# Kernel optimization log

Measured on AMD Instinct MI355X. Metric: run time of the kernel, lower is better.

## Reference

```python
import jax, jax.numpy as jnp
import numpy as np

T, B, TD, HD, VD = 64, 4096, 512, 256, 484
LN_EPS = 1e-5   # torch nn.LayerNorm default
COS_EPS = 1e-8  # torch F.cosine_similarity default


def setup_inputs() -> dict:
    key = jax.random.key(0)
    ks = jax.random.split(key, 6)
    w = lambda k, shape: jax.random.normal(k, shape, dtype=jnp.float32) * 0.02
    return {
        "t_feat": jax.random.normal(ks[0], (B, TD), dtype=jnp.float32),
        "W1": w(ks[1], (T, HD, TD)),            # torch Linear weight layout [out, in]
        "b1": w(ks[2], (T, HD)),
        "gamma": jnp.ones((T, HD), jnp.float32),
        "beta": jnp.zeros((T, HD), jnp.float32),
        "W2": w(ks[3], (T, VD, HD)),
        "b2": w(ks[4], (T, VD)),
        "centroids": jax.random.normal(ks[5], (T, VD), dtype=jnp.float32),
    }


def reference(t_feat, W1, b1, gamma, beta, W2, b2, centroids):
    # All T per-task mappers batched into one grouped GEMM pipeline.
    # Linear1: [B, TD] x [T, HD, TD] -> [T, B, HD]
    h = jnp.einsum("bd,thd->tbh", t_feat, W1) + b1[:, None, :]
    # LayerNorm over hidden dim (per task affine params)
    mu = jnp.mean(h, axis=-1, keepdims=True)
    var = jnp.mean(jnp.square(h - mu), axis=-1, keepdims=True)
    h = (h - mu) * jax.lax.rsqrt(var + LN_EPS) * gamma[:, None, :] + beta[:, None, :]
    # Exact GELU (torch nn.GELU default uses erf)
    h = jax.nn.gelu(h, approximate=False)
    # Linear2: [T, B, HD] x [T, VD, HD] -> [T, B, VD] predicted visual features
    v = jnp.einsum("tbh,tvh->tbv", h, W2) + b2[:, None, :]
    # Cosine similarity vs each task centroid (eps-clamped norms, as in torch)
    v_norm = jnp.maximum(jnp.linalg.norm(v, axis=-1), COS_EPS)          # [T, B]
    c_norm = jnp.maximum(jnp.linalg.norm(centroids, axis=-1), COS_EPS)  # [T]
    cos = jnp.einsum("tbv,tv->tb", v, centroids) / (v_norm * c_norm[:, None])
    distances = jnp.mean(1.0 - cos, axis=-1)  # [T] mean cosine distance per task
    best_task = jnp.argmin(distances)          # top-1 routing decision
    return distances, best_task
```

## Files before the change

kernel.cpp:

```cpp
#include <hip/hip_runtime.h>
#include <math.h>

#define TASKS 64
#define NB    4096
#define TDI   512
#define HDI   256
#define VDI   484

#define WS_TF   ((size_t)0)
#define WS_W1   ((size_t)4194304)
#define WS_W2   ((size_t)20971520)
#define WS_CN   ((size_t)37748736)
#define WS_BC   ((size_t)37748992)
#define WS_ACC  ((size_t)37749248)

#define LDS_HP 0
#define LDS_B2 32768
#define LDS_R0 34816
#define LDS_R1 35840
#define LDS_MU 36864
#define LDS_RS 37120
#define SMEM_BYTES 37376

typedef _Float16 half8 __attribute__((ext_vector_type(8)));
typedef float    f32x4 __attribute__((ext_vector_type(4)));

#define MFMA16(a, b, c) __builtin_amdgcn_mfma_f32_16x16x32_f16((a), (b), (c), 0, 0, 0)

__device__ __forceinline__ half8 cvt8(float4 v0, float4 v1) {
  half8 r;
  r[0]=(_Float16)v0.x; r[1]=(_Float16)v0.y; r[2]=(_Float16)v0.z; r[3]=(_Float16)v0.w;
  r[4]=(_Float16)v1.x; r[5]=(_Float16)v1.y; r[6]=(_Float16)v1.z; r[7]=(_Float16)v1.w;
  return r;
}

__device__ __forceinline__ float gelu_exact(float x) {
  float az = fabsf(x) * 0.70710678118654752f;
  float d  = fmaf(0.3275911f, az, 1.0f);
  float t; asm("v_rcp_f32 %0, %1" : "=v"(t) : "v"(d));
  float p  = fmaf(t, 1.061405429f, -1.453152027f);
  p = fmaf(t, p, 1.421413741f);
  p = fmaf(t, p, -0.284496736f);
  p = fmaf(t, p, 0.254829592f);
  p = p * t;
  float m = az * az * -1.4426950408889634f;
  float e; asm("v_exp_f32 %0, %1" : "=v"(e) : "v"(m));
  float er = fmaf(-p, e, 1.0f);
  er = copysignf(er, x);
  float hx = 0.5f * x;
  return fmaf(hx, er, hx);
}

extern "C" __global__ void prep_all(const float* __restrict__ t_feat,
                                    const float* __restrict__ W1,
                                    const float* __restrict__ W2,
                                    const float* __restrict__ b2,
                                    const float* __restrict__ cent,
                                    _Float16* __restrict__ tf,
                                    _Float16* __restrict__ w1,
                                    _Float16* __restrict__ w2,
                                    float* __restrict__ cnorm,
                                    float* __restrict__ bc,
                                    float* __restrict__ accum) {
  const int bid = blockIdx.x, tid = threadIdx.x;
  __shared__ float redc[256], redb[256];
  if (bid < 1024) {
    int p = bid * 256 + tid;
    int rb = p >> 12, r = p & 4095;
    int ks = r >> 8, rt = (r >> 6) & 3, q = (r >> 4) & 3, l15 = r & 15;
    int row = rb * 64 + rt * 16 + l15, k8 = ks * 4 + q;
    float4 v0 = ((const float4*)t_feat)[(row * 64 + k8) * 2];
    float4 v1 = ((const float4*)t_feat)[(row * 64 + k8) * 2 + 1];
    *(half8*)(tf + (size_t)p * 8) = cvt8(v0, v1);
  } else if (bid < 5120) {
    int p = (bid - 1024) * 256 + tid;
    int t = p >> 14, r = p & 16383;
    int w_ = r >> 12, ks = (r >> 8) & 15, ct = (r >> 6) & 3, q = (r >> 4) & 3, l15 = r & 15;
    int hd = w_ * 64 + ct * 16 + l15, k8 = ks * 4 + q;
    float4 v0 = ((const float4*)W1)[((size_t)(t * 256 + hd) * 64 + k8) * 2];
    float4 v1 = ((const float4*)W1)[((size_t)(t * 256 + hd) * 64 + k8) * 2 + 1];
    *(half8*)(w1 + (size_t)p * 8) = cvt8(v0, v1);
  } else if (bid < 9216) {
    int p = (bid - 5120) * 256 + tid;
    int t = p >> 14, r = p & 16383;
    int pass = r >> 13, w_ = (r >> 11) & 3, ks = (r >> 8) & 7;
    int ct = (r >> 6) & 3, q = (r >> 4) & 3, l15 = r & 15;
    int vd = pass * 256 + w_ * 64 + ct * 16 + l15, k8 = ks * 4 + q;
    half8 hv;
    if (vd < 484) {
      float4 v0 = ((const float4*)W2)[((size_t)(t * 484 + vd) * 64 + k8 * 2)];
      float4 v1 = ((const float4*)W2)[((size_t)(t * 484 + vd) * 64 + k8 * 2) + 1];
      hv = cvt8(v0, v1);
    } else if (vd >= 485) {
      #pragma unroll
      for (int i = 0; i < 8; ++i) hv[i] = (_Float16)0.f;
    } else {
      return;
    }
    *(half8*)(w2 + (size_t)p * 8) = hv;
  } else {
    int t = bid - 9216;
    int h = tid;
    float wcv = 0.f;
    for (int v = 0; v < VDI; ++v)
      wcv += W2[((size_t)t * VDI + v) * HDI + h] * cent[(size_t)t * VDI + v];
    {
      int ks = h >> 5, q = (h >> 3) & 3;
      size_t o = (size_t)t * 16384 + 8192 + 3 * 2048 + ks * 256 + 2 * 64 + q * 16 + 4;
      w2[o * 8 + (h & 7)] = (_Float16)wcv;
    }
    float c2 = 0.f, b2c = 0.f;
    for (int v = h; v < VDI; v += 256) {
      float c = cent[(size_t)t * VDI + v];
      c2 += c * c;
      b2c += b2[(size_t)t * VDI + v] * c;
    }
    redc[tid] = c2; redb[tid] = b2c;
    __syncthreads();
    if (tid < 64) {
      c2  = redc[tid] + redc[tid + 64] + redc[tid + 128] + redc[tid + 192];
      b2c = redb[tid] + redb[tid + 64] + redb[tid + 128] + redb[tid + 192];
      #pragma unroll
      for (int off = 32; off; off >>= 1) { c2 += __shfl_xor(c2, off); b2c += __shfl_xor(b2c, off); }
      if (tid == 0) { cnorm[t] = sqrtf(c2); bc[t] = b2c; accum[t] = 0.f; }
    }
  }
}


#define STEP_RELOAD(A, ACC, PB) do {                                           \
  __builtin_amdgcn_s_setprio(1);                                               \
  _Pragma("unroll") for (int ct_ = 0; ct_ < 4; ++ct_) {                        \
    ACC[0][ct_] = MFMA16(A[0], b[ct_], ACC[0][ct_]);                           \
    ACC[1][ct_] = MFMA16(A[1], b[ct_], ACC[1][ct_]);                           \
    ACC[2][ct_] = MFMA16(A[2], b[ct_], ACC[2][ct_]);                           \
    ACC[3][ct_] = MFMA16(A[3], b[ct_], ACC[3][ct_]);                           \
    b[ct_] = (PB)[ct_ * 64];                                                   \
  }                                                                            \
  __builtin_amdgcn_s_setprio(0);                                               \
} while (0)

#define STEP_LAST(A, ACC) do {                                                 \
  __builtin_amdgcn_s_setprio(1);                                               \
  _Pragma("unroll") for (int ct_ = 0; ct_ < 4; ++ct_) {                        \
    ACC[0][ct_] = MFMA16(A[0], b[ct_], ACC[0][ct_]);                           \
    ACC[1][ct_] = MFMA16(A[1], b[ct_], ACC[1][ct_]);                           \
    ACC[2][ct_] = MFMA16(A[2], b[ct_], ACC[2][ct_]);                           \
    ACC[3][ct_] = MFMA16(A[3], b[ct_], ACC[3][ct_]);                           \
  }                                                                            \
  __builtin_amdgcn_s_setprio(0);                                               \
} while (0)

#define LD_A4(D, P) do { D[0] = (P)[0]; D[1] = (P)[64]; D[2] = (P)[128]; D[3] = (P)[192]; } while (0)

extern "C" __global__ void __launch_bounds__(256, 4)
router_main(const half8* __restrict__ tfv,
            const half8* __restrict__ w1v,
            const half8* __restrict__ w2v,
            const float* __restrict__ b1,
            const float* __restrict__ gamma,
            const float* __restrict__ beta,
            const float* __restrict__ b2,
            const float* __restrict__ bc,
            const float* __restrict__ cnorm,
            float* __restrict__ accum) {
  __shared__ __align__(16) char smem[SMEM_BYTES];

  const int tid = threadIdx.x;
  const int bx  = blockIdx.x;
  const int t  = ((bx & 7) << 3) | (bx >> 9);
  const int rb = (bx >> 3) & 63;

  const int lane = tid & 63;
  const int w    = tid >> 6;
  const int quad = lane >> 4;
  const int l15  = lane & 15;

  f32x4 zero4 = {0.f, 0.f, 0.f, 0.f};
  f32x4 acc[4][4];
  #pragma unroll
  for (int rt = 0; rt < 4; ++rt)
    #pragma unroll
    for (int ct = 0; ct < 4; ++ct) acc[rt][ct] = zero4;

  half8 a0[4], a1[4], b[4];

  {
    const half8* pa = tfv + ((size_t)rb * 4096 + quad * 16 + l15);
    const half8* pb = w1v + ((size_t)t * 16384 + w * 4096 + quad * 16 + l15);
    LD_A4(a0, pa);
    b[0] = pb[0]; b[1] = pb[64]; b[2] = pb[128]; b[3] = pb[192];
    a1[0] = pa[256]; a1[1] = pa[320]; a1[2] = pa[384]; a1[3] = pa[448];
    pa += 512;
    pb += 256;
    #pragma unroll 1
    for (int ks = 0; ks < 14; ks += 2) {
      STEP_RELOAD(a0, acc, pb); pb += 256;
      LD_A4(a0, pa);            pa += 256;
      STEP_RELOAD(a1, acc, pb); pb += 256;
      LD_A4(a1, pa);            pa += 256;
    }
    STEP_RELOAD(a0, acc, pb);
    STEP_LAST(a1, acc);
  }

  float b1v[4], gv[4], bev[4];
  #pragma unroll
  for (int ct = 0; ct < 4; ++ct) {
    b1v[ct] = b1   [t * HDI + w * 64 + ct * 16 + l15];
    gv[ct]  = gamma[t * HDI + w * 64 + ct * 16 + l15];
    bev[ct] = beta [t * HDI + w * 64 + ct * 16 + l15];
  }
  {
    float* b2s = (float*)(smem + LDS_B2);
    int i0 = tid;
    b2s[i0] = (i0 < VDI) ? b2[(size_t)t * VDI + i0] : 0.f;
    int i1 = tid + 256;
    float v = 0.f;
    if (i1 < VDI) v = b2[(size_t)t * VDI + i1];
    else if (i1 == VDI) v = bc[t];
    b2s[i1] = v;
  }
  {
    float* red0 = (float*)(smem + LDS_R0);
    float* red1 = (float*)(smem + LDS_R1);
    #pragma unroll
    for (int rt = 0; rt < 4; ++rt)
      #pragma unroll
      for (int r = 0; r < 4; ++r) {
        float sv = 0.f, qv = 0.f;
        #pragma unroll
        for (int ct = 0; ct < 4; ++ct) {
          float v = acc[rt][ct][r] + b1v[ct];
          acc[rt][ct][r] = v;
          sv += v; qv += v * v;
        }
        sv += __shfl_xor(sv, 1); qv += __shfl_xor(qv, 1);
        sv += __shfl_xor(sv, 2); qv += __shfl_xor(qv, 2);
        sv += __shfl_xor(sv, 4); qv += __shfl_xor(qv, 4);
        sv += __shfl_xor(sv, 8); qv += __shfl_xor(qv, 8);
        if (l15 == 0) {
          int m = rt * 16 + quad * 4 + r;
          red0[w * 64 + m] = sv;
          red1[w * 64 + m] = qv;
        }
      }
    __syncthreads();
    if (tid < 64) {
      float s = red0[tid] + red0[64 + tid] + red0[128 + tid] + red0[192 + tid];
      float q = red1[tid] + red1[64 + tid] + red1[128 + tid] + red1[192 + tid];
      float mu = s * (1.f / HDI);
      float var = q * (1.f / HDI) - mu * mu;
      ((float*)(smem + LDS_MU))[tid] = mu;
      ((float*)(smem + LDS_RS))[tid] = rsqrtf(var + 1e-5f);
    }
    __syncthreads();
    const float* mus = (const float*)(smem + LDS_MU);
    const float* rss = (const float*)(smem + LDS_RS);
    #pragma unroll
    for (int rt = 0; rt < 4; ++rt)
      #pragma unroll
      for (int ct = 0; ct < 4; ++ct) {
        int col = w * 64 + ct * 16 + l15;
        int base = (((col >> 5) * 4 + rt) * 4 + ((col >> 3) & 3)) * 256
                 + quad * 64 + (l15 & 7) * 2;
        #pragma unroll
        for (int r = 0; r < 4; ++r) {
          int m = rt * 16 + quad * 4 + r;
          float x = (acc[rt][ct][r] - mus[m]) * rss[m];
          x = x * gv[ct] + bev[ct];
          float g = gelu_exact(x);
          *(_Float16*)(smem + LDS_HP + base + r * 16) = (_Float16)g;
        }
      }
    __syncthreads();
  }

  {
    const float* b2s = (const float*)(smem + LDS_B2);
    float* red0 = (float*)(smem + LDS_R0);
    float* red1 = (float*)(smem + LDS_R1);
    const char* ha = smem + LDS_HP + quad * 256 + l15 * 16;

    #pragma unroll 1
    for (int pass = 0; pass < 2; ++pass) {
      const half8* pc = w2v + ((size_t)t * 16384 + pass * 8192 + w * 2048 + quad * 16 + l15);
      f32x4 acc2[4][4];
      #pragma unroll
      for (int rt = 0; rt < 4; ++rt)
        #pragma unroll
        for (int ct = 0; ct < 4; ++ct) acc2[rt][ct] = zero4;

      a0[0] = *(const half8*)(ha);        a0[1] = *(const half8*)(ha + 1024);
      a0[2] = *(const half8*)(ha + 2048); a0[3] = *(const half8*)(ha + 3072);
      b[0] = pc[0]; b[1] = pc[64]; b[2] = pc[128]; b[3] = pc[192];
      a1[0] = *(const half8*)(ha + 4096); a1[1] = *(const half8*)(ha + 5120);
      a1[2] = *(const half8*)(ha + 6144); a1[3] = *(const half8*)(ha + 7168);
      pc += 256;
      #pragma unroll 1
      for (int ks = 0; ks < 6; ks += 2) {
        STEP_RELOAD(a0, acc2, pc); pc += 256;
        {
          const char* h2 = ha + (ks + 2) * 4096;
          a0[0] = *(const half8*)(h2);        a0[1] = *(const half8*)(h2 + 1024);
          a0[2] = *(const half8*)(h2 + 2048); a0[3] = *(const half8*)(h2 + 3072);
        }
        STEP_RELOAD(a1, acc2, pc); pc += 256;
        {
          const char* h3 = ha + (ks + 3) * 4096;
          a1[0] = *(const half8*)(h3);        a1[1] = *(const half8*)(h3 + 1024);
          a1[2] = *(const half8*)(h3 + 2048); a1[3] = *(const half8*)(h3 + 3072);
        }
      }
      STEP_RELOAD(a0, acc2, pc);
      STEP_LAST(a1, acc2);

      #pragma unroll
      for (int rt = 0; rt < 4; ++rt)
        #pragma unroll
        for (int r = 0; r < 4; ++r) {
          float ssq = 0.f, dtv = 0.f;
          #pragma unroll
          for (int ct = 0; ct < 4; ++ct) {
            int vcol = pass * 256 + w * 64 + ct * 16 + l15;
            float val = acc2[rt][ct][r] + b2s[vcol];
            ssq += (vcol < VDI) ? val * val : 0.f;
            dtv += (vcol == VDI) ? val : 0.f;
          }
          ssq += __shfl_xor(ssq, 1); dtv += __shfl_xor(dtv, 1);
          ssq += __shfl_xor(ssq, 2); dtv += __shfl_xor(dtv, 2);
          ssq += __shfl_xor(ssq, 4); dtv += __shfl_xor(dtv, 4);
          ssq += __shfl_xor(ssq, 8); dtv += __shfl_xor(dtv, 8);
          if (l15 == 0) {
            int m = rt * 16 + quad * 4 + r;
            if (pass == 0) {
              red0[w * 64 + m] = ssq;
            } else {
              red0[w * 64 + m] += ssq;
              red1[w * 64 + m] = dtv;
            }
          }
        }
    }

    __syncthreads();
    if (tid < 64) {
      float ss  = red0[tid] + red0[64 + tid] + red0[128 + tid] + red0[192 + tid];
      float dot = red1[tid] + red1[64 + tid] + red1[128 + tid] + red1[192 + tid];
      float cn = fmaxf(cnorm[t], 1e-8f);
      float vn = fmaxf(sqrtf(ss), 1e-8f);
      float part = 1.0f - dot / (vn * cn);
      part += __shfl_down(part, 32);
      part += __shfl_down(part, 16);
      part += __shfl_down(part, 8);
      part += __shfl_down(part, 4);
      part += __shfl_down(part, 2);
      part += __shfl_down(part, 1);
      if (tid == 0) atomicAdd(accum + t, part);
    }
  }
}

extern "C" __global__ void finalize_k(const float* __restrict__ accum, float* __restrict__ out) {
  int t = threadIdx.x;
  float d = accum[t] * (1.0f / (float)NB);
  out[t] = d;
  float bd = d; int bi = t;
  #pragma unroll
  for (int off = 32; off; off >>= 1) {
    float od = __shfl_xor(bd, off);
    int   oi = __shfl_xor(bi, off);
    if (od < bd || (od == bd && oi < bi)) { bd = od; bi = oi; }
  }
  if (t == 0) out[64] = (float)bi;
}

extern "C" void kernel_launch(void* const* d_in, const int* in_sizes, int n_in,
                              void* d_out, int out_size, void* d_ws, size_t ws_size,
                              hipStream_t stream) {
  const float* t_feat = (const float*)d_in[0];
  const float* W1     = (const float*)d_in[1];
  const float* b1     = (const float*)d_in[2];
  const float* gamma  = (const float*)d_in[3];
  const float* beta   = (const float*)d_in[4];
  const float* W2     = (const float*)d_in[5];
  const float* b2     = (const float*)d_in[6];
  const float* cent   = (const float*)d_in[7];

  char* ws = (char*)d_ws;
  _Float16* tf = (_Float16*)(ws + WS_TF);
  _Float16* w1 = (_Float16*)(ws + WS_W1);
  _Float16* w2 = (_Float16*)(ws + WS_W2);
  float* cnorm = (float*)(ws + WS_CN);
  float* bc    = (float*)(ws + WS_BC);
  float* accum = (float*)(ws + WS_ACC);
  float* out = (float*)d_out;

  prep_all<<<9280, 256, 0, stream>>>(t_feat, W1, W2, b2, cent,
                                     tf, w1, w2, cnorm, bc, accum);
  router_main<<<4096, 256, 0, stream>>>((const half8*)tf, (const half8*)w1, (const half8*)w2,
                                        b1, gamma, beta, b2, bc, cnorm, accum);
  finalize_k<<<1, 64, 0, stream>>>(accum, out);
}
```

Measured before the change: 344.5 us.

## Stage fp16 weight repacking through LDS and restructure second GEMM register pipeline

The prep kernel now converts fp32 inputs to fp16 by loading 64-row tiles into padded LDS with coalesced float4 reads, then writing them out in the MFMA fragment layout. This replaces scattered per-thread gathers and cuts the block count. In the main kernel, the gamma/beta/b2 loads move later so they overlap the LayerNorm reduction and fewer registers are live during GEMM1. GEMM2 switches from double-buffered A fragments to a single buffer whose reloads are interleaved with the MFMAs, lowering register pressure at the risk of exposing LDS latency.

```diff
diff --git a/kernel.cpp b/kernel.cpp
--- a/kernel.cpp
+++ b/kernel.cpp
@@ -26,13 +26,6 @@
 typedef float    f32x4 __attribute__((ext_vector_type(4)));
 
 #define MFMA16(a, b, c) __builtin_amdgcn_mfma_f32_16x16x32_f16((a), (b), (c), 0, 0, 0)
-
-__device__ __forceinline__ half8 cvt8(float4 v0, float4 v1) {
-  half8 r;
-  r[0]=(_Float16)v0.x; r[1]=(_Float16)v0.y; r[2]=(_Float16)v0.z; r[3]=(_Float16)v0.w;
-  r[4]=(_Float16)v1.x; r[5]=(_Float16)v1.y; r[6]=(_Float16)v1.z; r[7]=(_Float16)v1.w;
-  return r;
-}
 
 __device__ __forceinline__ float gelu_exact(float x) {
   float az = fabsf(x) * 0.70710678118654752f;
@@ -62,45 +55,64 @@
                                     float* __restrict__ cnorm,
                                     float* __restrict__ bc,
                                     float* __restrict__ accum) {
+  __shared__ __align__(16) char pbuf[17408];
   const int bid = blockIdx.x, tid = threadIdx.x;
-  __shared__ float redc[256], redb[256];
-  if (bid < 1024) {
-    int p = bid * 256 + tid;
-    int rb = p >> 12, r = p & 4095;
-    int ks = r >> 8, rt = (r >> 6) & 3, q = (r >> 4) & 3, l15 = r & 15;
-    int row = rb * 64 + rt * 16 + l15, k8 = ks * 4 + q;
-    float4 v0 = ((const float4*)t_feat)[(row * 64 + k8) * 2];
-    float4 v1 = ((const float4*)t_feat)[(row * 64 + k8) * 2 + 1];
-    *(half8*)(tf + (size_t)p * 8) = cvt8(v0, v1);
-  } else if (bid < 5120) {
-    int p = (bid - 1024) * 256 + tid;
-    int t = p >> 14, r = p & 16383;
-    int w_ = r >> 12, ks = (r >> 8) & 15, ct = (r >> 6) & 3, q = (r >> 4) & 3, l15 = r & 15;
-    int hd = w_ * 64 + ct * 16 + l15, k8 = ks * 4 + q;
-    float4 v0 = ((const float4*)W1)[((size_t)(t * 256 + hd) * 64 + k8) * 2];
-    float4 v1 = ((const float4*)W1)[((size_t)(t * 256 + hd) * 64 + k8) * 2 + 1];
-    *(half8*)(w1 + (size_t)p * 8) = cvt8(v0, v1);
-  } else if (bid < 9216) {
-    int p = (bid - 5120) * 256 + tid;
-    int t = p >> 14, r = p & 16383;
-    int pass = r >> 13, w_ = (r >> 11) & 3, ks = (r >> 8) & 7;
-    int ct = (r >> 6) & 3, q = (r >> 4) & 3, l15 = r & 15;
-    int vd = pass * 256 + w_ * 64 + ct * 16 + l15, k8 = ks * 4 + q;
-    half8 hv;
-    if (vd < 484) {
-      float4 v0 = ((const float4*)W2)[((size_t)(t * 484 + vd) * 64 + k8 * 2)];
-      float4 v1 = ((const float4*)W2)[((size_t)(t * 484 + vd) * 64 + k8 * 2) + 1];
-      hv = cvt8(v0, v1);
-    } else if (vd >= 485) {
-      #pragma unroll
-      for (int i = 0; i < 8; ++i) hv[i] = (_Float16)0.f;
+
+  if (bid < 2304) {
+    const float* src;
+    half8* dst;
+    int w2vdBase = -1;
+
+    if (bid < 256) {
+      int rb = bid >> 2, kq = bid & 3;
+      src = t_feat + (size_t)rb * 64 * 512 + kq * 128;
+      dst = (half8*)tf + ((size_t)rb * 4096 + kq * 1024);
+    } else if (bid < 1280) {
+      int g = bid - 256;
+      int t = g >> 4, w_ = (g >> 2) & 3, kq = g & 3;
+      src = W1 + ((size_t)t * 256 + w_ * 64) * 512 + kq * 128;
+      dst = (half8*)w1 + ((size_t)t * 16384 + w_ * 4096 + kq * 1024);
     } else {
-      return;
-    }
-    *(half8*)(w2 + (size_t)p * 8) = hv;
+      int g = bid - 1280;
+      int t = g >> 4, sub = g & 15;
+      int p = sub >> 3, w_ = (sub >> 1) & 3, kq = sub & 1;
+      src = W2 + (size_t)t * 484 * 256 + kq * 128;
+      w2vdBase = p * 256 + w_ * 64;
+      dst = (half8*)w2 + ((size_t)t * 16384 + p * 8192 + w_ * 2048 + kq * 1024);
+    }
+
+    const int srcStride = (w2vdBase < 0) ? 512 : 256;
+    ushort* lds = (ushort*)pbuf;
+    #pragma unroll
+    for (int j = 0; j < 8; ++j) {
+      int f = j * 256 + tid;
+      int row = f >> 5, kc = f & 31;
+      float4 v = make_float4(0.f, 0.f, 0.f, 0.f);
+      if (w2vdBase < 0) {
+        v = ((const float4*)(src + (size_t)row * srcStride))[kc];
+      } else {
+        int vd = w2vdBase + row;
+        if (vd < VDI) v = ((const float4*)(src + (size_t)vd * 256))[kc];
+      }
+      _Float16 h4[4] = {(_Float16)v.x, (_Float16)v.y, (_Float16)v.z, (_Float16)v.w};
+      *(ushort4*)(&lds[row * 136 + kc * 4]) = *(const ushort4*)h4;
+    }
+    __syncthreads();
+
+    #pragma unroll
+    for (int j = 0; j < 4; ++j) {
+      int u = j * 256 + tid;
+      int ksl = u >> 8, rg = (u >> 6) & 3, q = (u >> 4) & 3, l15 = u & 15;
+      int row = rg * 16 + l15, k8l = ksl * 4 + q;
+      half8 val = *(const half8*)(pbuf + row * 272 + k8l * 16);
+      if (w2vdBase >= 0 && (w2vdBase + row) == VDI) continue;
+      dst[u] = val;
+    }
   } else {
-    int t = bid - 9216;
+    int t = bid - 2304;
     int h = tid;
+    float* redc = (float*)pbuf;
+    float* redb = (float*)(pbuf + 1024);
     float wcv = 0.f;
     for (int v = 0; v < VDI; ++v)
       wcv += W2[((size_t)t * VDI + v) * HDI + h] * cent[(size_t)t * VDI + v];
@@ -152,6 +164,25 @@
 } while (0)
 
 #define LD_A4(D, P) do { D[0] = (P)[0]; D[1] = (P)[64]; D[2] = (P)[128]; D[3] = (P)[192]; } while (0)
+
+#define P3_STEP(ACC, HN) do {                                                  \
+  __builtin_amdgcn_s_setprio(1);                                               \
+  ACC[0][0]=MFMA16(a0[0],b[0],ACC[0][0]); ACC[1][0]=MFMA16(a0[1],b[0],ACC[1][0]); \
+  ACC[2][0]=MFMA16(a0[2],b[0],ACC[2][0]); ACC[3][0]=MFMA16(a0[3],b[0],ACC[3][0]); \
+  b[0]=pc[0];                                                                  \
+  ACC[0][1]=MFMA16(a0[0],b[1],ACC[0][1]); ACC[1][1]=MFMA16(a0[1],b[1],ACC[1][1]); \
+  ACC[2][1]=MFMA16(a0[2],b[1],ACC[2][1]); ACC[3][1]=MFMA16(a0[3],b[1],ACC[3][1]); \
+  b[1]=pc[64];                                                                 \
+  ACC[0][2]=MFMA16(a0[0],b[2],ACC[0][2]); ACC[1][2]=MFMA16(a0[1],b[2],ACC[1][2]); \
+  ACC[2][2]=MFMA16(a0[2],b[2],ACC[2][2]); ACC[3][2]=MFMA16(a0[3],b[2],ACC[3][2]); \
+  b[2]=pc[128];                                                                \
+  ACC[0][3]=MFMA16(a0[0],b[3],ACC[0][3]); a0[0]=*(const half8*)(HN);           \
+  ACC[1][3]=MFMA16(a0[1],b[3],ACC[1][3]); a0[1]=*(const half8*)((HN)+1024);    \
+  ACC[2][3]=MFMA16(a0[2],b[3],ACC[2][3]); a0[2]=*(const half8*)((HN)+2048);    \
+  ACC[3][3]=MFMA16(a0[3],b[3],ACC[3][3]); a0[3]=*(const half8*)((HN)+3072);    \
+  b[3]=pc[192]; pc+=256;                                                       \
+  __builtin_amdgcn_s_setprio(0);                                               \
+} while (0)
 
 extern "C" __global__ void __launch_bounds__(256, 4)
 router_main(const half8* __restrict__ tfv,
@@ -204,23 +235,10 @@
     STEP_LAST(a1, acc);
   }
 
-  float b1v[4], gv[4], bev[4];
+  float b1v[4];
   #pragma unroll
-  for (int ct = 0; ct < 4; ++ct) {
-    b1v[ct] = b1   [t * HDI + w * 64 + ct * 16 + l15];
-    gv[ct]  = gamma[t * HDI + w * 64 + ct * 16 + l15];
-    bev[ct] = beta [t * HDI + w * 64 + ct * 16 + l15];
-  }
-  {
-    float* b2s = (float*)(smem + LDS_B2);
-    int i0 = tid;
-    b2s[i0] = (i0 < VDI) ? b2[(size_t)t * VDI + i0] : 0.f;
-    int i1 = tid + 256;
-    float v = 0.f;
-    if (i1 < VDI) v = b2[(size_t)t * VDI + i1];
-    else if (i1 == VDI) v = bc[t];
-    b2s[i1] = v;
-  }
+  for (int ct = 0; ct < 4; ++ct)
+    b1v[ct] = b1[t * HDI + w * 64 + ct * 16 + l15];
   {
     float* red0 = (float*)(smem + LDS_R0);
     float* red1 = (float*)(smem + LDS_R1);
@@ -254,11 +272,33 @@
       ((float*)(smem + LDS_MU))[tid] = mu;
       ((float*)(smem + LDS_RS))[tid] = rsqrtf(var + 1e-5f);
     }
+    float gvv[4], bevv[4];
+    #pragma unroll
+    for (int ct = 0; ct < 4; ++ct) {
+      gvv[ct]  = gamma[t * HDI + w * 64 + ct * 16 + l15];
+      bevv[ct] = beta [t * HDI + w * 64 + ct * 16 + l15];
+    }
+    {
+      float* b2s = (float*)(smem + LDS_B2);
+      int i0 = tid;
+      b2s[i0] = (i0 < VDI) ? b2[(size_t)t * VDI + i0] : 0.f;
+      int i1 = tid + 256;
+      float v = 0.f;
+      if (i1 < VDI) v = b2[(size_t)t * VDI + i1];
+      else if (i1 == VDI) v = bc[t];
+      b2s[i1] = v;
+    }
     __syncthreads();
     const float* mus = (const float*)(smem + LDS_MU);
     const float* rss = (const float*)(smem + LDS_RS);
     #pragma unroll
-    for (int rt = 0; rt < 4; ++rt)
+    for (int rt = 0; rt < 4; ++rt) {
+      float m4[4], s4[4];
+      #pragma unroll
+      for (int r = 0; r < 4; ++r) {
+        int m = rt * 16 + quad * 4 + r;
+        m4[r] = mus[m]; s4[r] = rss[m];
+      }
       #pragma unroll
       for (int ct = 0; ct < 4; ++ct) {
         int col = w * 64 + ct * 16 + l15;
@@ -266,13 +306,12 @@
                  + quad * 64 + (l15 & 7) * 2;
         #pragma unroll
         for (int r = 0; r < 4; ++r) {
-          int m = rt * 16 + quad * 4 + r;
-          float x = (acc[rt][ct][r] - mus[m]) * rss[m];
-          x = x * gv[ct] + bev[ct];
-          float g = gelu_exact(x);
-          *(_Float16*)(smem + LDS_HP + base + r * 16) = (_Float16)g;
+          float x = (acc[rt][ct][r] - m4[r]) * s4[r];
+          x = x * gvv[ct] + bevv[ct];
+          *(_Float16*)(smem + LDS_HP + base + r * 16) = (_Float16)gelu_exact(x);
         }
       }
+    }
     __syncthreads();
   }
 
@@ -294,26 +333,12 @@
       a0[0] = *(const half8*)(ha);        a0[1] = *(const half8*)(ha + 1024);
       a0[2] = *(const half8*)(ha + 2048); a0[3] = *(const half8*)(ha + 3072);
       b[0] = pc[0]; b[1] = pc[64]; b[2] = pc[128]; b[3] = pc[192];
-      a1[0] = *(const half8*)(ha + 4096); a1[1] = *(const half8*)(ha + 5120);
-      a1[2] = *(const half8*)(ha + 6144); a1[3] = *(const half8*)(ha + 7168);
       pc += 256;
       #pragma unroll 1
-      for (int ks = 0; ks < 6; ks += 2) {
-        STEP_RELOAD(a0, acc2, pc); pc += 256;
-        {
-          const char* h2 = ha + (ks + 2) * 4096;
-          a0[0] = *(const half8*)(h2);        a0[1] = *(const half8*)(h2 + 1024);
-          a0[2] = *(const half8*)(h2 + 2048); a0[3] = *(const half8*)(h2 + 3072);
-        }
-        STEP_RELOAD(a1, acc2, pc); pc += 256;
-        {
-          const char* h3 = ha + (ks + 3) * 4096;
-          a1[0] = *(const half8*)(h3);        a1[1] = *(const half8*)(h3 + 1024);
-          a1[2] = *(const half8*)(h3 + 2048); a1[3] = *(const half8*)(h3 + 3072);
-        }
+      for (int ks = 0; ks < 7; ++ks) {
+        P3_STEP(acc2, ha + (ks + 1) * 4096);
       }
-      STEP_RELOAD(a0, acc2, pc);
-      STEP_LAST(a1, acc2);
+      STEP_LAST(a0, acc2);
 
       #pragma unroll
       for (int rt = 0; rt < 4; ++rt)
@@ -396,7 +421,7 @@
   float* accum = (float*)(ws + WS_ACC);
   float* out = (float*)d_out;
 
-  prep_all<<<9280, 256, 0, stream>>>(t_feat, W1, W2, b2, cent,
+  prep_all<<<2368, 256, 0, stream>>>(t_feat, W1, W2, b2, cent,
                                      tf, w1, w2, cnorm, bc, accum);
   router_main<<<4096, 256, 0, stream>>>((const half8*)tf, (const half8*)w1, (const half8*)w2,
                                         b1, gamma, beta, b2, bc, cnorm, accum);
```

After: 317.9 us. -7.7%, faster.
